# Performance work log

Measured on AMD Instinct MI355X. Metric: run time of the kernel, lower is better.

The kernel has to match this reference:

```python
import jax, jax.numpy as jnp
import numpy as np

B, T, C = 4, 2048, 2048
H = 16
D = C // H  # 128


def setup_inputs() -> dict:
    key = jax.random.key(0)
    k1, k2, k3, k4 = jax.random.split(key, 4)
    x = jax.random.normal(k1, (B, T, C), dtype=jnp.float32)
    rope_freqs = jax.random.uniform(k2, (D // 2,), dtype=jnp.float32)
    # torch Linear weights: (out_features, in_features)
    W_attn = jax.random.normal(k3, (3 * C, C), dtype=jnp.float32) * (1.0 / np.sqrt(C))
    W_proj = jax.random.normal(k4, (C, C), dtype=jnp.float32) * (1.0 / np.sqrt(C))
    return {"x": x, "rope_freqs": rope_freqs, "W_attn": W_attn, "W_proj": W_proj}


def _apply_rope(q, k, rope_freqs):
    # q, k: (B, H, T, D); rope_freqs: (D//2,)
    S = q.shape[2]
    positions = jnp.arange(S, dtype=q.dtype)[:, None]            # (S, 1)
    theta = positions * rope_freqs[None, :]                       # (S, D//2)
    sin_t = jnp.sin(theta)[None, None]                            # (1,1,S,D//2)
    cos_t = jnp.cos(theta)[None, None]
    q1, q2 = q[..., 0::2], q[..., 1::2]
    k1, k2 = k[..., 0::2], k[..., 1::2]
    q_out = jnp.concatenate([q1 * cos_t - q2 * sin_t, q1 * sin_t + q2 * cos_t], axis=-1)
    k_out = jnp.concatenate([k1 * cos_t - k2 * sin_t, k1 * sin_t + k2 * cos_t], axis=-1)
    return q_out, k_out


def reference(x, rope_freqs, W_attn, W_proj):
    b, t, c = x.shape
    qkv = jnp.einsum('btc,fc->btf', x, W_attn)                    # (B,T,3C)
    q, k, v = jnp.split(qkv, 3, axis=-1)
    q = q.reshape(b, t, H, D).transpose(0, 2, 1, 3)               # (B,H,T,D)
    k = k.reshape(b, t, H, D).transpose(0, 2, 1, 3)
    v = v.reshape(b, t, H, D).transpose(0, 2, 1, 3)
    q, k = _apply_rope(q, k, rope_freqs)
    scale = 1.0 / jnp.sqrt(jnp.asarray(D, dtype=x.dtype))
    scores = jnp.einsum('bhqd,bhkd->bhqk', q, k) * scale          # (B,H,T,T)
    causal = jnp.tril(jnp.ones((t, t), dtype=bool))
    scores = jnp.where(causal[None, None], scores, jnp.asarray(-jnp.inf, dtype=scores.dtype))
    probs = jax.nn.softmax(scores, axis=-1)
    y = jnp.einsum('bhqk,bhkd->bhqd', probs, v)                   # (B,H,T,D)
    y = y.transpose(0, 2, 1, 3).reshape(b, t, c)
    return jnp.einsum('btc,fc->btf', y, W_proj)
```

## Files before the change

### kernel.cpp

```cpp
#include <hip/hip_runtime.h>
#include <cstdint>
#include <cstddef>


typedef unsigned short u16;
typedef u16    u16x8 __attribute__((ext_vector_type(8)));
typedef __bf16 bf16x8 __attribute__((ext_vector_type(8)));
typedef float  f32x4 __attribute__((ext_vector_type(4)));

#define MFMA16(a, b, c) __builtin_amdgcn_mfma_f32_16x16x32_bf16( \
    __builtin_bit_cast(bf16x8, (a)), __builtin_bit_cast(bf16x8, (b)), (c), 0, 0, 0)

static __device__ __forceinline__ u16 f2b(float f) {
  unsigned u = __builtin_bit_cast(unsigned, f);
  unsigned r = (u + 0x7FFFu + ((u >> 16) & 1u)) >> 16;
  return (u16)r;
}

static __device__ __forceinline__ void gld_lds16(const void* g, void* l) {
  __builtin_amdgcn_global_load_lds(
      (__attribute__((address_space(1))) unsigned int*)(void*)(g),
      (__attribute__((address_space(3))) unsigned int*)(l),
      16, 0, 0);
}

#define BARRIER() asm volatile("s_barrier" ::: "memory")
#define LGKM0()   do { asm volatile("s_waitcnt lgkmcnt(0)" ::: "memory"); \
                       __builtin_amdgcn_sched_barrier(0); } while (0)
#define WAIT_VM(n) asm volatile("s_waitcnt vmcnt(" #n ")" ::: "memory")

__global__ __launch_bounds__(256) void cvt_bf16(const float4* __restrict__ src,
                                                u16x8* __restrict__ dst, int n8) {
  int i = blockIdx.x * 256 + threadIdx.x;
  if (i >= n8) return;
  float4 a = src[i * 2], b = src[i * 2 + 1];
  u16x8 o;
  o[0] = f2b(a.x); o[1] = f2b(a.y); o[2] = f2b(a.z); o[3] = f2b(a.w);
  o[4] = f2b(b.x); o[5] = f2b(b.y); o[6] = f2b(b.z); o[7] = f2b(b.w);
  dst[i] = o;
}

static __device__ __forceinline__ void rdA(u16x8 (&af)[4][2], const u16* p,
                                           int cx0, int cx1) {
#pragma unroll
  for (int i = 0; i < 4; ++i) {
    af[i][0] = *(const u16x8*)(p + i * 1024 + cx0);
    af[i][1] = *(const u16x8*)(p + i * 1024 + cx1);
  }
}

static __device__ __forceinline__ void rdB(u16x8 (&bf)[2][2], const u16* p,
                                           int cx0, int cx1) {
#pragma unroll
  for (int j = 0; j < 2; ++j) {
    bf[j][0] = *(const u16x8*)(p + j * 1024 + cx0);
    bf[j][1] = *(const u16x8*)(p + j * 1024 + cx1);
  }
}

static __device__ __forceinline__ void mm16(f32x4 (&acc)[8][4], int ib, int jb,
                                            const u16x8 (&af)[4][2],
                                            const u16x8 (&bf)[2][2]) {
#pragma unroll
  for (int i = 0; i < 4; ++i)
#pragma unroll
    for (int j = 0; j < 2; ++j) {
      acc[ib + i][jb + j] = MFMA16(af[i][0], bf[j][0], acc[ib + i][jb + j]);
      acc[ib + i][jb + j] = MFMA16(af[i][1], bf[j][1], acc[ib + i][jb + j]);
    }
}

static __device__ __forceinline__ void gemm256_main(
    const u16* __restrict__ A, const u16* __restrict__ Bw, int K,
    int m0, int n0, u16* sm, f32x4 (&acc)[8][4]) {
  const int tid = threadIdx.x;
  const int lane = tid & 63, wv = tid >> 6;
  const int quad = lane >> 4, col = lane & 15;
  const int wm = wv >> 2, wn = wv & 3;

  u16* LA0 = sm;
  u16* LB0 = sm + 16384;
  u16* LA1 = sm + 32768;
  u16* LB1 = sm + 49152;

#pragma unroll
  for (int i = 0; i < 8; ++i)
#pragma unroll
    for (int j = 0; j < 4; ++j) acc[i][j] = (f32x4){0.f, 0.f, 0.f, 0.f};

  const int r8 = lane >> 3, ch = lane & 7;
  const int sc8 = (ch ^ r8) << 3;
  const u16 *aS[4], *bS[4];
  int dof[4];
#pragma unroll
  for (int u = 0; u < 4; ++u) {
    int row = u * 64 + wv * 8 + r8;
    aS[u] = A + (size_t)(m0 + row) * K + sc8;
    bS[u] = Bw + (size_t)(n0 + row) * K + sc8;
    dof[u] = (u * 64 + wv * 8) * 64;
  }

  const int cx0 = ((quad) ^ (col & 7)) << 3;
  const int cx1 = ((4 | quad) ^ (col & 7)) << 3;
  const int offA = (wm * 128 + col) * 64;
  const int offB = (wn * 64 + col) * 64;

  gld_lds16(bS[0], LB0 + dof[0]); gld_lds16(bS[1], LB0 + dof[1]);
  gld_lds16(bS[2], LB0 + dof[2]); gld_lds16(bS[3], LB0 + dof[3]);
  gld_lds16(aS[0], LA0 + dof[0]); gld_lds16(aS[2], LA0 + dof[2]);
  gld_lds16(aS[1], LA0 + dof[1]); gld_lds16(aS[3], LA0 + dof[3]);
  WAIT_VM(2);
  BARRIER();

  u16x8 af[4][2], bfL[2][2], bfH[2][2];
  const int nIt = K >> 7;
#pragma unroll 1
  for (int it = 0; it < nIt; ++it) {
    const size_t ko = (size_t)it * 128 + 64;
    const size_t kn = (size_t)it * 128 + 128;
    const bool hn = (it + 1 < nIt);

    rdA(af, LA0 + offA, cx0, cx1);
    rdB(bfL, LB0 + offB, cx0, cx1);
    gld_lds16(bS[0] + ko, LB1 + dof[0]); gld_lds16(bS[1] + ko, LB1 + dof[1]);
    BARRIER(); LGKM0();
    __builtin_amdgcn_s_setprio(1); mm16(acc, 0, 0, af, bfL);
    __builtin_amdgcn_s_setprio(0);
    BARRIER();
    rdB(bfH, LB0 + offB + 2048, cx0, cx1);
    gld_lds16(bS[2] + ko, LB1 + dof[2]); gld_lds16(bS[3] + ko, LB1 + dof[3]);
    WAIT_VM(4);
    BARRIER(); LGKM0();
    __builtin_amdgcn_s_setprio(1); mm16(acc, 0, 2, af, bfH);
    __builtin_amdgcn_s_setprio(0);
    BARRIER();
    rdA(af, LA0 + offA + 4096, cx0, cx1);
    gld_lds16(aS[0] + ko, LA1 + dof[0]); gld_lds16(aS[2] + ko, LA1 + dof[2]);
    BARRIER(); LGKM0();
    __builtin_amdgcn_s_setprio(1); mm16(acc, 4, 0, af, bfL);
    __builtin_amdgcn_s_setprio(0);
    BARRIER();
    gld_lds16(aS[1] + ko, LA1 + dof[1]); gld_lds16(aS[3] + ko, LA1 + dof[3]);
    WAIT_VM(2);
    BARRIER(); __builtin_amdgcn_sched_barrier(0);
    __builtin_amdgcn_s_setprio(1); mm16(acc, 4, 2, af, bfH);
    __builtin_amdgcn_s_setprio(0);
    BARRIER();
    rdA(af, LA1 + offA, cx0, cx1);
    rdB(bfL, LB1 + offB, cx0, cx1);
    if (hn) { gld_lds16(bS[0] + kn, LB0 + dof[0]); gld_lds16(bS[1] + kn, LB0 + dof[1]); }
    BARRIER(); LGKM0();
    __builtin_amdgcn_s_setprio(1); mm16(acc, 0, 0, af, bfL);
    __builtin_amdgcn_s_setprio(0);
    BARRIER();
    rdB(bfH, LB1 + offB + 2048, cx0, cx1);
    if (hn) {
      gld_lds16(bS[2] + kn, LB0 + dof[2]); gld_lds16(bS[3] + kn, LB0 + dof[3]);
      WAIT_VM(4);
    } else {
      WAIT_VM(0);
    }
    BARRIER(); LGKM0();
    __builtin_amdgcn_s_setprio(1); mm16(acc, 0, 2, af, bfH);
    __builtin_amdgcn_s_setprio(0);
    BARRIER();
    rdA(af, LA1 + offA + 4096, cx0, cx1);
    if (hn) { gld_lds16(aS[0] + kn, LA0 + dof[0]); gld_lds16(aS[2] + kn, LA0 + dof[2]); }
    BARRIER(); LGKM0();
    __builtin_amdgcn_s_setprio(1); mm16(acc, 4, 0, af, bfL);
    __builtin_amdgcn_s_setprio(0);
    BARRIER();
    if (hn) { gld_lds16(aS[1] + kn, LA0 + dof[1]); gld_lds16(aS[3] + kn, LA0 + dof[3]); }
    WAIT_VM(2);
    BARRIER(); __builtin_amdgcn_sched_barrier(0);
    __builtin_amdgcn_s_setprio(1); mm16(acc, 4, 2, af, bfH);
    __builtin_amdgcn_s_setprio(0);
    BARRIER();
  }
}

__global__ __launch_bounds__(512, 2) void gemm_qkv(
    const u16* __restrict__ A, const u16* __restrict__ Bw,
    const float* __restrict__ freqs, int K,
    u16* __restrict__ Qp, u16* __restrict__ Kp, u16* __restrict__ Vp) {
  extern __shared__ u16 sm[];
  const int bid = blockIdx.x;
  const int x = bid & 7, o = bid >> 3;
  const int rnd = o >> 5, w = o & 31;
  const int m0 = (x * 4 + (w & 3)) * 256;
  const int n0 = (rnd * 8 + (w >> 2)) * 256;

  f32x4 acc[8][4];
  gemm256_main(A, Bw, K, m0, n0, sm, acc);

  const int tid = threadIdx.x;
  const int lane = tid & 63, wv = tid >> 6;
  const int quad = lane >> 4, col = lane & 15;
  const int wm = wv >> 2, wn = wv & 3;

  const int which = n0 >> 11;
  const int h0 = (n0 & 2047) >> 7;
  const int b = m0 >> 11, t0 = m0 & 2047;
  const int hl = wn >> 1;


  if (which == 2) {
#pragma unroll
    for (int j = 0; j < 4; ++j) {
      int d = (wn & 1) * 64 + j * 16 + col;
      int key = (d >> 1) & 7;
#pragma unroll
      for (int i = 0; i < 8; ++i) {
        int tbase = wm * 128 + i * 16 + quad * 4;
        int reg = hl * 4 + (tbase >> 6);
        int tc0 = tbase & 63;
        u16* d0 = sm + reg * 8192 + d * 64 + ((((tc0 >> 3) ^ key)) << 3) + (tc0 & 7);
        *(unsigned*)d0 = (unsigned)f2b(acc[i][j][0]) |
                         ((unsigned)f2b(acc[i][j][1]) << 16);
        *(unsigned*)(d0 + 2) = (unsigned)f2b(acc[i][j][2]) |
                               ((unsigned)f2b(acc[i][j][3]) << 16);
      }
    }
    __syncthreads();
#pragma unroll
    for (int s = 0; s < 16; ++s) {
      int cch = tid + (s << 9);
      int reg = cch >> 10, ci = cch & 1023;
      int d = ci >> 3, cc = ci & 7;
      u16x8 v = *(const u16x8*)(sm + reg * 8192 + d * 64 +
                                (((cc ^ ((d >> 1) & 7))) << 3));
      int hh = reg >> 2, ktg = reg & 3;
      int kt = (t0 >> 6) + ktg;
      size_t off = (((size_t)((b * 16 + h0 + hh) * 32 + kt)) << 13) +
                   (size_t)d * 64 + (cc << 3);
      *(u16x8*)(Vp + off) = v;
    }
  } else {
    u16* dst = (which == 0) ? Qp : Kp;
    const bool evenlane = (col & 1) == 0;
    const int rlo = evenlane ? 0 : 2;
#pragma unroll
    for (int j = 0; j < 4; ++j) {
      int dd = (wn & 1) * 64 + j * 16 + col;
      int jj = dd >> 1;
      float fr = freqs[jj];
#pragma unroll
      for (int i = 0; i < 8; ++i) {
        float oth[4];
#pragma unroll
        for (int r = 0; r < 4; ++r) oth[r] = __shfl_xor(acc[i][j][r], 1);
#pragma unroll
        for (int rr = 0; rr < 2; ++rr) {
          int r = rlo + rr;
          float q1 = evenlane ? acc[i][j][r] : oth[r];
          float q2 = evenlane ? oth[r] : acc[i][j][r];
          int tgl = wm * 128 + i * 16 + quad * 4 + r;
          int t = t0 + tgl;
          float theta = (float)t * fr;
          float rev = theta * 0.15915494309189535f;
          rev -= floorf(rev);
          float sn = __builtin_amdgcn_sinf(rev);
          float cs = __builtin_amdgcn_cosf(rev);
          unsigned pk = (unsigned)f2b(q1 * cs - q2 * sn) |
                        ((unsigned)f2b(q1 * sn + q2 * cs) << 16);
          int row = hl * 256 + tgl;
          int sc = (jj >> 2) ^ (row & 15);
          *(unsigned*)(sm + row * 128 + (sc << 3) + 2 * (jj & 3)) = pk;
        }
      }
    }
    __syncthreads();
#pragma unroll
    for (int s = 0; s < 16; ++s) {
      int cch = tid + (s << 9);
      int row = cch >> 4, cc = cch & 15;
      u16x8 v = *(const u16x8*)(sm + row * 128 + ((cc ^ (row & 15)) << 3));
      int hh = row >> 8, tl = row & 255;
      size_t off = ((size_t)((b * 16 + h0 + hh) * 2048 + t0 + tl)) * 128 +
                   (cc << 3);
      *(u16x8*)(dst + off) = v;
    }
  }
}

__global__ __launch_bounds__(512, 2) void gemm_proj(
    const u16* __restrict__ A, const u16* __restrict__ Bw,
    int N, int K, float* __restrict__ out) {
  extern __shared__ u16 sm[];
  const int m0 = blockIdx.y * 256, n0 = blockIdx.x * 256;

  f32x4 acc[8][4];
  gemm256_main(A, Bw, K, m0, n0, sm, acc);

  const int tid = threadIdx.x;
  const int lane = tid & 63, wv = tid >> 6;
  const int quad = lane >> 4, col = lane & 15;
  const int wm = wv >> 2, wn = wv & 3;

#pragma unroll
  for (int i = 0; i < 8; ++i) {
    int mg = m0 + wm * 128 + i * 16 + quad * 4;
#pragma unroll
    for (int j = 0; j < 4; ++j) {
      int ng = n0 + wn * 64 + j * 16 + col;
#pragma unroll
      for (int r = 0; r < 4; ++r) out[(size_t)(mg + r) * N + ng] = acc[i][j][r];
    }
  }
}

__global__ __launch_bounds__(512, 4) void fattn(
    const u16* __restrict__ Qb, const u16* __restrict__ Kb, const u16* __restrict__ Vt,
    u16* __restrict__ Yb) {
  extern __shared__ u16 smem[];
  u16* lP = smem + 32768 + (threadIdx.x >> 6) * 1024;

  const int tid = threadIdx.x;
  const int lane = tid & 63, wv = tid >> 6;
  const int quad = lane >> 4, col = lane & 15;
  const int bh = blockIdx.x;
  const int p = blockIdx.y;
  const int b = bh >> 4, h = bh & 15;
  const size_t base = (size_t)bh << 18;
  const float kcomb = 0.08838834764831845f * 1.4426950408889634f;

  const u16* srcBase;
  u16* ldsBase;
  int so[4], lo[4];
  if (wv < 4) {
    srcBase = Kb + base;
    ldsBase = smem;
#pragma unroll
    for (int u = 0; u < 4; ++u) {
      int row = wv * 16 + u * 4 + (lane >> 4);
      int sc = (lane & 15) ^ (row & 15);
      so[u] = row * 128 + (sc << 3);
      lo[u] = (wv * 16 + u * 4) * 128;
    }
  } else {
    int vw = wv - 4;
    srcBase = Vt + base;
    ldsBase = smem + 16384;
#pragma unroll
    for (int u = 0; u < 4; ++u) {
      int row = vw * 32 + u * 8 + (lane >> 3);
      int sc = (lane & 7) ^ (row & 7);
      so[u] = row * 64 + (sc << 3);
      lo[u] = (vw * 32 + u * 8) * 64;
    }
  }

#define FA_STAGE(KT, BI)                                                        \
    do {                                                                        \
      const u16* s_ = srcBase + (size_t)(KT) * 8192;                            \
      u16* d_ = ldsBase + (BI) * 8192;                                          \
      gld_lds16(s_ + so[0], d_ + lo[0]); gld_lds16(s_ + so[1], d_ + lo[1]);     \
      gld_lds16(s_ + so[2], d_ + lo[2]); gld_lds16(s_ + so[3], d_ + lo[3]);     \
    } while (0)

#pragma unroll 1
  for (int phase = 0; phase < 2; ++phase) {
    const int tq = phase ? (15 - p) : p;
    const int qr0 = tq * 128 + wv * 16;
    const int dkt = qr0 >> 6;

    u16x8 qf[4];
#pragma unroll
    for (int t = 0; t < 4; ++t)
      qf[t] = *(const u16x8*)(Qb + base + (size_t)(qr0 + col) * 128 + t * 32 + quad * 8);

    f32x4 mrow = (f32x4){-1e30f, -1e30f, -1e30f, -1e30f};
    f32x4 lrow = (f32x4){0.f, 0.f, 0.f, 0.f};
    f32x4 o[8];
#pragma unroll
    for (int dt = 0; dt < 8; ++dt) o[dt] = (f32x4){0.f, 0.f, 0.f, 0.f};

    const int nkt = 2 * tq + 2;

    FA_STAGE(0, 0);
    WAIT_VM(0);
    BARRIER();

#pragma unroll 1
    for (int kt = 0; kt < nkt; ++kt) {
      const int cur = kt & 1;
      if (kt + 1 < nkt) {
        FA_STAGE(kt + 1, cur ^ 1);
        WAIT_VM(4);
      } else {
        WAIT_VM(0);
      }
      BARRIER();

      if (kt <= dkt) {
        const u16* lK = smem + cur * 8192;
        const u16* lVt = smem + 16384 + cur * 8192;
        f32x4 sv[4];
#pragma unroll
        for (int nt = 0; nt < 4; ++nt) {
          f32x4 s = (f32x4){0.f, 0.f, 0.f, 0.f};
#pragma unroll
          for (int t = 0; t < 4; ++t) {
            int krow = nt * 16 + col;
            u16x8 kf = *(const u16x8*)&lK[krow * 128 + ((((t << 2) | quad) ^ (krow & 15)) << 3)];
            s = MFMA16(qf[t], kf, s);
          }
          sv[nt] = s;
        }
#pragma unroll
        for (int nt = 0; nt < 4; ++nt)
#pragma unroll
          for (int r = 0; r < 4; ++r) sv[nt][r] *= kcomb;
        if (kt == dkt) {
#pragma unroll
          for (int nt = 0; nt < 4; ++nt) {
            int cg = kt * 64 + nt * 16 + col;
#pragma unroll
            for (int r = 0; r < 4; ++r)
              if (cg > qr0 + quad * 4 + r) sv[nt][r] = -1e30f;
          }
        }
        f32x4 mx = sv[0];
#pragma unroll
        for (int nt = 1; nt < 4; ++nt)
#pragma unroll
          for (int r = 0; r < 4; ++r) mx[r] = fmaxf(mx[r], sv[nt][r]);
#pragma unroll
        for (int off = 1; off < 16; off <<= 1)
#pragma unroll
          for (int r = 0; r < 4; ++r) mx[r] = fmaxf(mx[r], __shfl_xor(mx[r], off));
        f32x4 alpha;
#pragma unroll
        for (int r = 0; r < 4; ++r) {
          float mn = fmaxf(mrow[r], mx[r]);
          alpha[r] = exp2f(mrow[r] - mn);
          mrow[r] = mn;
        }
        f32x4 ps = (f32x4){0.f, 0.f, 0.f, 0.f};
#pragma unroll
        for (int nt = 0; nt < 4; ++nt)
#pragma unroll
          for (int r = 0; r < 4; ++r) {
            float pe = exp2f(sv[nt][r] - mrow[r]);
            ps[r] += pe;
            int row = quad * 4 + r;
            int chn = ((nt << 1) | (col >> 3)) ^ (row & 7);
            lP[row * 64 + (chn << 3) + (col & 7)] = f2b(pe);
          }
#pragma unroll
        for (int off = 1; off < 16; off <<= 1)
#pragma unroll
          for (int r = 0; r < 4; ++r) ps[r] += __shfl_xor(ps[r], off);
#pragma unroll
        for (int r = 0; r < 4; ++r) lrow[r] = lrow[r] * alpha[r] + ps[r];
#pragma unroll
        for (int dt = 0; dt < 8; ++dt)
#pragma unroll
          for (int r = 0; r < 4; ++r) o[dt][r] *= alpha[r];
#pragma unroll
        for (int t = 0; t < 2; ++t) {
          u16x8 pf = *(const u16x8*)&lP[col * 64 + ((((t << 2) | quad) ^ (col & 7)) << 3)];
#pragma unroll
          for (int dt = 0; dt < 8; ++dt) {
            int drow = dt * 16 + col;
            u16x8 vf = *(const u16x8*)&lVt[drow * 64 + ((((t << 2) | quad) ^ (drow & 7)) << 3)];
            o[dt] = MFMA16(pf, vf, o[dt]);
          }
        }
      }
      BARRIER();
    }

    f32x4 inv;
#pragma unroll
    for (int r = 0; r < 4; ++r) inv[r] = 1.0f / lrow[r];
#pragma unroll
    for (int dt = 0; dt < 8; ++dt)
#pragma unroll
      for (int r = 0; r < 4; ++r) {
        float y = o[dt][r] * inv[r];
        int q = qr0 + quad * 4 + r;
        Yb[((size_t)(b * 2048 + q)) * 2048 + h * 128 + dt * 16 + col] = f2b(y);
      }
  }
#undef FA_STAGE
}

extern "C" void kernel_launch(void* const* d_in, const int* in_sizes, int n_in,
                              void* d_out, int out_size, void* d_ws, size_t ws_size,
                              hipStream_t stream) {
  (void)in_sizes; (void)n_in; (void)out_size; (void)ws_size;
  const float* x     = (const float*)d_in[0];
  const float* freqs = (const float*)d_in[1];
  const float* Wattn = (const float*)d_in[2];
  const float* Wproj = (const float*)d_in[3];
  float* out = (float*)d_out;
  char* ws = (char*)d_ws;

  u16* Wq_b = (u16*)(ws + 0);
  u16* Wp_b = (u16*)(ws + 25165824);
  u16* x_b  = (u16*)(ws + 33554432);
  u16* Qb   = (u16*)(ws + 67108864);
  u16* Kb   = (u16*)(ws + 100663296);
  u16* Vt   = (u16*)(ws + 134217728);
  u16* Yb   = (u16*)(ws + 167772160);

  static bool attr_done = false;
  if (!attr_done) {
    (void)hipFuncSetAttribute((const void*)gemm_qkv,
                              hipFuncAttributeMaxDynamicSharedMemorySize, 131072);
    (void)hipFuncSetAttribute((const void*)gemm_proj,
                              hipFuncAttributeMaxDynamicSharedMemorySize, 131072);
    (void)hipFuncSetAttribute((const void*)fattn,
                              hipFuncAttributeMaxDynamicSharedMemorySize, 81920);
    attr_done = true;
  }

  cvt_bf16<<<6144, 256, 0, stream>>>((const float4*)Wattn, (u16x8*)Wq_b, 12582912 / 8);
  cvt_bf16<<<2048, 256, 0, stream>>>((const float4*)Wproj, (u16x8*)Wp_b, 4194304 / 8);
  cvt_bf16<<<8192, 256, 0, stream>>>((const float4*)x, (u16x8*)x_b, 16777216 / 8);

  gemm_qkv<<<dim3(768), 512, 131072, stream>>>(x_b, Wq_b, freqs, 2048, Qb, Kb, Vt);
  fattn<<<dim3(64, 8), 512, 81920, stream>>>(Qb, Kb, Vt, Yb);
  gemm_proj<<<dim3(8, 32), 512, 131072, stream>>>(Yb, Wp_b, 2048, 2048, out);
}
```

Before: 585.8 us.

## Single-buffer attention K/V in static LDS, add lazy rescale and MFMA priority

Replaces the double-buffered dynamic-LDS K/V pipeline in the attention kernel with a single static buffer loaded synchronously each iteration between two barriers. The LDS footprint shrinks from 80 KB to 48 KB, which may let more blocks stay resident per CU. It also skips the online-softmax rescale of the output and row sum when no row's max grows by more than 8 (in log2 units), and raises wave priority around the MFMA sections. The cost is that global-to-LDS loads no longer overlap compute within a block, and the lazy rescale lets unnormalised values grow by up to 2^8.

```diff
diff --git a/kernel.cpp b/kernel.cpp
--- a/kernel.cpp
+++ b/kernel.cpp
@@ -312,8 +312,9 @@
 __global__ __launch_bounds__(512, 4) void fattn(
     const u16* __restrict__ Qb, const u16* __restrict__ Kb, const u16* __restrict__ Vt,
     u16* __restrict__ Yb) {
-  extern __shared__ u16 smem[];
-  u16* lP = smem + 32768 + (threadIdx.x >> 6) * 1024;
+  __shared__ alignas(16) u16 lK[64 * 128];
+  __shared__ alignas(16) u16 lV[128 * 64];
+  __shared__ alignas(16) u16 lPs[8][16 * 64];
 
   const int tid = threadIdx.x;
   const int lane = tid & 63, wv = tid >> 6;
@@ -323,39 +324,39 @@
   const int b = bh >> 4, h = bh & 15;
   const size_t base = (size_t)bh << 18;
   const float kcomb = 0.08838834764831845f * 1.4426950408889634f;
+  u16* lP = lPs[wv];
 
   const u16* srcBase;
-  u16* ldsBase;
-  int so[4], lo[4];
+  u16* dA0; u16* dA1; u16* dA2; u16* dA3;
+  int so[4];
   if (wv < 4) {
     srcBase = Kb + base;
-    ldsBase = smem;
 #pragma unroll
     for (int u = 0; u < 4; ++u) {
       int row = wv * 16 + u * 4 + (lane >> 4);
       int sc = (lane & 15) ^ (row & 15);
       so[u] = row * 128 + (sc << 3);
-      lo[u] = (wv * 16 + u * 4) * 128;
-    }
+    }
+    dA0 = lK + (wv * 16 + 0) * 128; dA1 = lK + (wv * 16 + 4) * 128;
+    dA2 = lK + (wv * 16 + 8) * 128; dA3 = lK + (wv * 16 + 12) * 128;
   } else {
     int vw = wv - 4;
     srcBase = Vt + base;
-    ldsBase = smem + 16384;
 #pragma unroll
     for (int u = 0; u < 4; ++u) {
       int row = vw * 32 + u * 8 + (lane >> 3);
       int sc = (lane & 7) ^ (row & 7);
       so[u] = row * 64 + (sc << 3);
-      lo[u] = (vw * 32 + u * 8) * 64;
-    }
-  }
-
-#define FA_STAGE(KT, BI)                                                        \
+    }
+    dA0 = lV + (vw * 32 + 0) * 64;  dA1 = lV + (vw * 32 + 8) * 64;
+    dA2 = lV + (vw * 32 + 16) * 64; dA3 = lV + (vw * 32 + 24) * 64;
+  }
+
+#define FA_STAGE(KT)                                                            \
     do {                                                                        \
       const u16* s_ = srcBase + (size_t)(KT) * 8192;                            \
-      u16* d_ = ldsBase + (BI) * 8192;                                          \
-      gld_lds16(s_ + so[0], d_ + lo[0]); gld_lds16(s_ + so[1], d_ + lo[1]);     \
-      gld_lds16(s_ + so[2], d_ + lo[2]); gld_lds16(s_ + so[3], d_ + lo[3]);     \
+      gld_lds16(s_ + so[0], dA0); gld_lds16(s_ + so[1], dA1);                   \
+      gld_lds16(s_ + so[2], dA2); gld_lds16(s_ + so[3], dA3);                   \
     } while (0)
 
 #pragma unroll 1
@@ -376,26 +377,15 @@
     for (int dt = 0; dt < 8; ++dt) o[dt] = (f32x4){0.f, 0.f, 0.f, 0.f};
 
     const int nkt = 2 * tq + 2;
-
-    FA_STAGE(0, 0);
-    WAIT_VM(0);
-    BARRIER();
-
 #pragma unroll 1
     for (int kt = 0; kt < nkt; ++kt) {
-      const int cur = kt & 1;
-      if (kt + 1 < nkt) {
-        FA_STAGE(kt + 1, cur ^ 1);
-        WAIT_VM(4);
-      } else {
-        WAIT_VM(0);
-      }
-      BARRIER();
+      __syncthreads();
+      FA_STAGE(kt);
+      __syncthreads();
 
       if (kt <= dkt) {
-        const u16* lK = smem + cur * 8192;
-        const u16* lVt = smem + 16384 + cur * 8192;
         f32x4 sv[4];
+        __builtin_amdgcn_s_setprio(1);
 #pragma unroll
         for (int nt = 0; nt < 4; ++nt) {
           f32x4 s = (f32x4){0.f, 0.f, 0.f, 0.f};
@@ -407,6 +397,7 @@
           }
           sv[nt] = s;
         }
+        __builtin_amdgcn_s_setprio(0);
 #pragma unroll
         for (int nt = 0; nt < 4; ++nt)
 #pragma unroll
@@ -429,12 +420,21 @@
         for (int off = 1; off < 16; off <<= 1)
 #pragma unroll
           for (int r = 0; r < 4; ++r) mx[r] = fmaxf(mx[r], __shfl_xor(mx[r], off));
-        f32x4 alpha;
-#pragma unroll
-        for (int r = 0; r < 4; ++r) {
-          float mn = fmaxf(mrow[r], mx[r]);
-          alpha[r] = exp2f(mrow[r] - mn);
-          mrow[r] = mn;
+        bool cheap = (mx[0] - mrow[0] <= 8.f) & (mx[1] - mrow[1] <= 8.f) &
+                     (mx[2] - mrow[2] <= 8.f) & (mx[3] - mrow[3] <= 8.f);
+        if (!__all(cheap)) {
+          f32x4 alpha;
+#pragma unroll
+          for (int r = 0; r < 4; ++r) {
+            float mn = fmaxf(mrow[r], mx[r]);
+            alpha[r] = exp2f(mrow[r] - mn);
+            mrow[r] = mn;
+            lrow[r] *= alpha[r];
+          }
+#pragma unroll
+          for (int dt = 0; dt < 8; ++dt)
+#pragma unroll
+            for (int r = 0; r < 4; ++r) o[dt][r] *= alpha[r];
         }
         f32x4 ps = (f32x4){0.f, 0.f, 0.f, 0.f};
 #pragma unroll
@@ -452,23 +452,20 @@
 #pragma unroll
           for (int r = 0; r < 4; ++r) ps[r] += __shfl_xor(ps[r], off);
 #pragma unroll
-        for (int r = 0; r < 4; ++r) lrow[r] = lrow[r] * alpha[r] + ps[r];
-#pragma unroll
-        for (int dt = 0; dt < 8; ++dt)
-#pragma unroll
-          for (int r = 0; r < 4; ++r) o[dt][r] *= alpha[r];
+        for (int r = 0; r < 4; ++r) lrow[r] += ps[r];
+        __builtin_amdgcn_s_setprio(1);
 #pragma unroll
         for (int t = 0; t < 2; ++t) {
           u16x8 pf = *(const u16x8*)&lP[col * 64 + ((((t << 2) | quad) ^ (col & 7)) << 3)];
 #pragma unroll
           for (int dt = 0; dt < 8; ++dt) {
             int drow = dt * 16 + col;
-            u16x8 vf = *(const u16x8*)&lVt[drow * 64 + ((((t << 2) | quad) ^ (drow & 7)) << 3)];
+            u16x8 vf = *(const u16x8*)&lV[drow * 64 + ((((t << 2) | quad) ^ (drow & 7)) << 3)];
             o[dt] = MFMA16(pf, vf, o[dt]);
           }
         }
+        __builtin_amdgcn_s_setprio(0);
       }
-      BARRIER();
     }
 
     f32x4 inv;
@@ -511,8 +508,6 @@
                               hipFuncAttributeMaxDynamicSharedMemorySize, 131072);
     (void)hipFuncSetAttribute((const void*)gemm_proj,
                               hipFuncAttributeMaxDynamicSharedMemorySize, 131072);
-    (void)hipFuncSetAttribute((const void*)fattn,
-                              hipFuncAttributeMaxDynamicSharedMemorySize, 81920);
     attr_done = true;
   }
 
@@ -521,6 +516,6 @@
   cvt_bf16<<<8192, 256, 0, stream>>>((const float4*)x, (u16x8*)x_b, 16777216 / 8);
 
   gemm_qkv<<<dim3(768), 512, 131072, stream>>>(x_b, Wq_b, freqs, 2048, Qb, Kb, Vt);
-  fattn<<<dim3(64, 8), 512, 81920, stream>>>(Qb, Kb, Vt, Yb);
+  fattn<<<dim3(64, 8), 512, 0, stream>>>(Qb, Kb, Vt, Yb);
   gemm_proj<<<dim3(8, 32), 512, 131072, stream>>>(Yb, Wp_b, 2048, 2048, out);
 }
```

New measurement: 583.2 us. About the same (-0.4%).
